# Optimization experiments

Hardware: AMD Instinct MI355X
Metric: run time of the kernel (lower is better)

## Reference

```python
import jax, jax.numpy as jnp
import numpy as np

D_MODEL = 1024
NUM_HEADS = 16
D_K = D_MODEL // NUM_HEADS
B, S = 2, 2048


def setup_inputs() -> dict:
    key = jax.random.key(0)
    ks = jax.random.split(key, 12)
    s = 1.0 / np.sqrt(D_MODEL)
    return {
        "query": jax.random.normal(ks[0], (B, S, D_MODEL), jnp.float32),
        "key": jax.random.normal(ks[1], (B, S, D_MODEL), jnp.float32),
        "value": jax.random.normal(ks[2], (B, S, D_MODEL), jnp.float32),
        "mask": jnp.ones((B, S), jnp.int32),
        "Wq": jax.random.uniform(ks[3], (D_MODEL, D_MODEL), jnp.float32, -s, s),
        "bq": jax.random.uniform(ks[4], (D_MODEL,), jnp.float32, -s, s),
        "Wk": jax.random.uniform(ks[5], (D_MODEL, D_MODEL), jnp.float32, -s, s),
        "bk": jax.random.uniform(ks[6], (D_MODEL,), jnp.float32, -s, s),
        "Wv": jax.random.uniform(ks[7], (D_MODEL, D_MODEL), jnp.float32, -s, s),
        "bv": jax.random.uniform(ks[8], (D_MODEL,), jnp.float32, -s, s),
        "Wo": jax.random.uniform(ks[9], (D_MODEL, D_MODEL), jnp.float32, -s, s),
        "bo": jax.random.uniform(ks[10], (D_MODEL,), jnp.float32, -s, s),
    }


def reference(query, key, value, mask, Wq, bq, Wk, bk, Wv, bv, Wo, bo):
    b, s, _ = query.shape
    scale = jnp.sqrt(jnp.asarray(D_K, jnp.float32)).astype(query.dtype)
    # QKV projections: x @ W.T + b (torch nn.Linear convention)
    Q = (query @ Wq.T + bq).reshape(b, s, NUM_HEADS, D_K).transpose(0, 2, 1, 3)
    K = (key @ Wk.T + bk).reshape(b, -1, NUM_HEADS, D_K).transpose(0, 2, 1, 3)
    V = (value @ Wv.T + bv).reshape(b, -1, NUM_HEADS, D_K).transpose(0, 2, 1, 3)
    # scores in fp32, then cast back to input dtype (matches source)
    scores = jnp.einsum('bhqd,bhkd->bhqk', Q.astype(jnp.float32), K.astype(jnp.float32)) / scale
    scores = scores.astype(Q.dtype)
    # 2D mask [B,S] -> [B,1,1,S], broadcast over heads/queries
    fill = jnp.finfo(scores.dtype).min
    scores = jnp.where(mask[:, None, None, :] == 0, fill, scores)
    attn = jax.nn.softmax(scores, axis=-1)  # dropout p=0 -> identity
    context = jnp.einsum('bhqk,bhkd->bhqd', attn, V)
    context = context.transpose(0, 2, 1, 3).reshape(b, s, D_MODEL)
    return context @ Wo.T + bo
```

## Files before the change

kernel.cpp:

```cpp
#include <hip/hip_runtime.h>


typedef __bf16 bf16_8 __attribute__((ext_vector_type(8)));
typedef float  f32x4  __attribute__((ext_vector_type(4)));
typedef float  f32x16 __attribute__((ext_vector_type(16)));
typedef unsigned int u32x4 __attribute__((ext_vector_type(4)));

#define MFMA16(a, b, c) __builtin_amdgcn_mfma_f32_16x16x32_bf16((a), (b), (c), 0, 0, 0)
#define MFMA32(a, b, c) __builtin_amdgcn_mfma_f32_32x32x16_bf16((a), (b), (c), 0, 0, 0)

__device__ __forceinline__ void async_ld16(const void* g, void* l) {
  __builtin_amdgcn_global_load_lds(
      (__attribute__((address_space(1))) void*)g,
      (__attribute__((address_space(3))) void*)l, 16, 0, 0);
}

__device__ __forceinline__ void gemm_core_128(
    const __bf16* __restrict__ A, const __bf16* __restrict__ BT, int K,
    int tm, int tn, __bf16* At, __bf16* Bt, f32x4 acc[4][4]) {
  const int tid  = threadIdx.x;
  const int lane = tid & 63;
  const int w    = tid >> 6;
  const int quad = lane >> 4;
  const int c16  = lane & 15;
  const int wm = w >> 1, wn = w & 1;

  const int ch0  = w * 2;
  const int row0 = ch0 * 16 + (lane >> 2);
  const int col0 = (lane & 3) * 8;
  const __bf16* Ag = A  + (size_t)(tm + row0) * K + col0;
  const __bf16* Bg = BT + (size_t)(tn + row0) * K + col0;
  __bf16* Al = At + ch0 * 512;
  __bf16* Bl = Bt + ch0 * 512;
  const size_t rowK16 = (size_t)16 * K;

  for (int kt = 0; kt < K; kt += 32) {
    async_ld16(Ag + kt,          Al);
    async_ld16(Ag + rowK16 + kt, Al + 512);
    async_ld16(Bg + kt,          Bl);
    async_ld16(Bg + rowK16 + kt, Bl + 512);
    __syncthreads();

    bf16_8 af[4], bfr[4];
#pragma unroll
    for (int mi = 0; mi < 4; ++mi)
      af[mi] = *(const bf16_8*)(At + (wm * 64 + mi * 16 + c16) * 32 + quad * 8);
#pragma unroll
    for (int ni = 0; ni < 4; ++ni)
      bfr[ni] = *(const bf16_8*)(Bt + (wn * 64 + ni * 16 + c16) * 32 + quad * 8);
#pragma unroll
    for (int mi = 0; mi < 4; ++mi)
#pragma unroll
      for (int ni = 0; ni < 4; ++ni)
        acc[mi][ni] = MFMA16(af[mi], bfr[ni], acc[mi][ni]);
    __syncthreads();
  }
}

__global__ __launch_bounds__(256)
void qkv_fused(const __bf16* __restrict__ xq, const __bf16* __restrict__ xk,
               const __bf16* __restrict__ xv,
               const __bf16* __restrict__ wq, const __bf16* __restrict__ wk,
               const __bf16* __restrict__ wv,
               const float* __restrict__ bq, const float* __restrict__ bk,
               const float* __restrict__ bv,
               __bf16* __restrict__ Qo, __bf16* __restrict__ Ko,
               __bf16* __restrict__ Vo) {
  __shared__ __bf16 At[128 * 32];
  __shared__ __bf16 Bt[128 * 32];
  const int z  = blockIdx.z;
  const int bx = blockIdx.x;
  const __bf16 *A, *BT;
  const float* bias;
  int tm, tn;
  if (z == 2) {
    A = wv; BT = xv; bias = bv;
    tm = (bx >> 5) * 128; tn = (bx & 31) * 128;
  } else if (z == 1) {
    A = xk; BT = wk; bias = bk;
    tm = (bx >> 3) * 128; tn = (bx & 7) * 128;
  } else {
    A = xq; BT = wq; bias = bq;
    tm = (bx >> 3) * 128; tn = (bx & 7) * 128;
  }

  f32x4 acc[4][4];
  const f32x4 zero4 = {0.f, 0.f, 0.f, 0.f};
#pragma unroll
  for (int i = 0; i < 4; ++i)
#pragma unroll
    for (int j = 0; j < 4; ++j) acc[i][j] = zero4;

  gemm_core_128(A, BT, 1024, tm, tn, At, Bt, acc);

  const int lane = threadIdx.x & 63;
  const int w    = threadIdx.x >> 6;
  const int quad = lane >> 4, c16 = lane & 15;
  const int wm = w >> 1, wn = w & 1;

  if (z == 2) {
#pragma unroll
    for (int mi = 0; mi < 4; ++mi) {
#pragma unroll
      for (int ni = 0; ni < 4; ++ni) {
        const int n  = tn + wn * 64 + ni * 16 + c16;
        const int bb = n >> 11, s = n & 2047;
#pragma unroll
        for (int r = 0; r < 4; ++r) {
          const int m  = tm + wm * 64 + mi * 16 + quad * 4 + r;
          const int hh = m >> 6, d = m & 63;
          Vo[(((size_t)(bb * 16 + hh) * 64 + d) << 11) + s] =
              (__bf16)(acc[mi][ni][r] + bias[m]);
        }
      }
    }
  } else {
    __bf16* Out = (z == 1) ? Ko : Qo;
    const float scale = (z == 0) ? 0.125f : 1.0f;
#pragma unroll
    for (int mi = 0; mi < 4; ++mi) {
#pragma unroll
      for (int ni = 0; ni < 4; ++ni) {
        const int n  = tn + wn * 64 + ni * 16 + c16;
        const int hh = n >> 6, d = n & 63;
        const float bn = bias[n];
#pragma unroll
        for (int r = 0; r < 4; ++r) {
          const int m  = tm + wm * 64 + mi * 16 + quad * 4 + r;
          const int bb = m >> 11, s = m & 2047;
          Out[(((size_t)(bb * 16 + hh) * 2048 + s) << 6) + d] =
              (__bf16)((acc[mi][ni][r] + bn) * scale);
        }
      }
    }
  }
}

__global__ __launch_bounds__(256)
void out_proj(const __bf16* __restrict__ ctx, const __bf16* __restrict__ wo,
              const float* __restrict__ bo, float* __restrict__ out) {
  __shared__ __bf16 At[64 * 32];
  __shared__ __bf16 Bt[128 * 32];
  const int bx = blockIdx.x;
  const int tm = (bx >> 3) * 64, tn = (bx & 7) * 128;

  const int tid  = threadIdx.x;
  const int lane = tid & 63, w = tid >> 6;
  const int quad = lane >> 4, c16 = lane & 15;
  const int wm = w >> 1, wn = w & 1;

  const int row0 = lane >> 2, col0 = (lane & 3) * 8;
  const __bf16* Ag = ctx + (size_t)(tm + w * 16 + row0) * 1024 + col0;
  const __bf16* Bg = wo  + (size_t)(tn + w * 32 + row0) * 1024 + col0;
  __bf16* Al = At + w * 512;
  __bf16* Bl = Bt + w * 1024;

  f32x4 acc[2][4];
  const f32x4 zero4 = {0.f, 0.f, 0.f, 0.f};
#pragma unroll
  for (int i = 0; i < 2; ++i)
#pragma unroll
    for (int j = 0; j < 4; ++j) acc[i][j] = zero4;

  for (int kt = 0; kt < 1024; kt += 32) {
    async_ld16(Ag + kt, Al);
    async_ld16(Bg + kt, Bl);
    async_ld16(Bg + 16 * 1024 + kt, Bl + 512);
    __syncthreads();

    bf16_8 af[2], bfr[4];
#pragma unroll
    for (int mi = 0; mi < 2; ++mi)
      af[mi] = *(const bf16_8*)(At + (wm * 32 + mi * 16 + c16) * 32 + quad * 8);
#pragma unroll
    for (int ni = 0; ni < 4; ++ni)
      bfr[ni] = *(const bf16_8*)(Bt + (wn * 64 + ni * 16 + c16) * 32 + quad * 8);
#pragma unroll
    for (int mi = 0; mi < 2; ++mi)
#pragma unroll
      for (int ni = 0; ni < 4; ++ni)
        acc[mi][ni] = MFMA16(af[mi], bfr[ni], acc[mi][ni]);
    __syncthreads();
  }

#pragma unroll
  for (int mi = 0; mi < 2; ++mi) {
#pragma unroll
    for (int ni = 0; ni < 4; ++ni) {
      const int n = tn + wn * 64 + ni * 16 + c16;
      const float bn = bo[n];
#pragma unroll
      for (int r = 0; r < 4; ++r) {
        const int m = tm + wm * 32 + mi * 16 + quad * 4 + r;
        out[(size_t)m * 1024 + n] = acc[mi][ni][r] + bn;
      }
    }
  }
}

__global__ __launch_bounds__(512, 4)
void flash_attn(const __bf16* __restrict__ Qg, const __bf16* __restrict__ Kg,
                const __bf16* __restrict__ VTg, const int* __restrict__ maskg,
                __bf16* __restrict__ ctx) {
  __shared__ __align__(16) __bf16 Kl[2][64 * 72];
  __shared__ __align__(16) __bf16 Vl[2][64 * 72];
  __shared__ __align__(16) float  maskadd[2][64];
  __shared__ __align__(16) float  Om[4][32][64];
  __shared__ float Lm[4][32];

  const int t    = threadIdx.x;
  const int lane = t & 63;
  const int w    = t >> 6;
  const int g    = w & 3;
  const int hh   = w >> 2;
  const int n32  = lane & 31;
  const int h    = lane >> 5;

  const int linear = blockIdx.x + (blockIdx.y << 4) + (blockIdx.z << 8);
  const int sw     = (linear & 7) * 64 + (linear >> 3);
  const int qt     = sw & 15;
  const int head   = (sw >> 4) & 15;
  const int b      = sw >> 8;

  const size_t bh = (size_t)(b * 16 + head);
  const int qbase = qt * 128 + g * 32;

  bf16_8 bq[4];
  {
    const __bf16* qptr = Qg + (bh * 2048 + qbase + n32) * 64 + h * 8;
#pragma unroll
    for (int s = 0; s < 4; ++s) bq[s] = *(const bf16_8*)(qptr + s * 16);
  }

  const f32x16 z16 = {0.f,0.f,0.f,0.f,0.f,0.f,0.f,0.f,
                      0.f,0.f,0.f,0.f,0.f,0.f,0.f,0.f};
  f32x16 o0 = z16, o1 = z16;
  float lsum = 0.f;

  const int tl   = t & 255;
  const int srow = tl >> 2, scc = (tl & 3) * 16;
  const __bf16* Kgp = Kg  + (bh * 2048 + hh * 1024) * 64;
  const __bf16* Vgp = VTg + bh * 64 * 2048 + hh * 1024;
  const int*    mgp = maskg + b * 2048 + hh * 1024;
  const float LOG2E = 1.44269504088896f;

  for (int kt = 0; kt < 1024; kt += 64) {
    {
      const size_t kb = (size_t)(kt + srow) * 64 + scc;
      *(bf16_8*)&Kl[hh][srow * 72 + scc]     = *(const bf16_8*)&Kgp[kb];
      *(bf16_8*)&Kl[hh][srow * 72 + scc + 8] = *(const bf16_8*)&Kgp[kb + 8];
      const size_t vbi = (size_t)srow * 2048 + kt + scc;
      *(bf16_8*)&Vl[hh][srow * 72 + scc]     = *(const bf16_8*)&Vgp[vbi];
      *(bf16_8*)&Vl[hh][srow * 72 + scc + 8] = *(const bf16_8*)&Vgp[vbi + 8];
      if (tl < 64) maskadd[hh][tl] = mgp[kt + tl] ? -17.3123404907f : -1e30f;
    }
    __syncthreads();

#pragma unroll
    for (int kt2 = 0; kt2 < 2; ++kt2) {
      f32x16 p = z16;
#pragma unroll
      for (int s = 0; s < 4; ++s) {
        const bf16_8 ka =
            *(const bf16_8*)&Kl[hh][(kt2 * 32 + n32) * 72 + s * 16 + h * 8];
        p = MFMA32(ka, bq[s], p);
      }
      unsigned c[8];
#pragma unroll
      for (int i = 0; i < 8; ++i) {
        const int r0 = 2 * i, r1 = 2 * i + 1;
        const float ma0 =
            maskadd[hh][kt2 * 32 + (r0 & 3) + 8 * (r0 >> 2) + 4 * h];
        const float ma1 =
            maskadd[hh][kt2 * 32 + (r1 & 3) + 8 * (r1 >> 2) + 4 * h];
        const float e0 = __builtin_amdgcn_exp2f(fmaf(p[r0], LOG2E, ma0));
        const float e1 = __builtin_amdgcn_exp2f(fmaf(p[r1], LOG2E, ma1));
        lsum += e0 + e1;
        union { __bf16 hx[2]; unsigned u; } uu;
        uu.hx[0] = (__bf16)e0;
        uu.hx[1] = (__bf16)e1;
        c[i] = uu.u;
      }
      asm volatile("v_permlane32_swap_b32 %0, %1" : "+v"(c[0]), "+v"(c[2]));
      asm volatile("v_permlane32_swap_b32 %0, %1" : "+v"(c[1]), "+v"(c[3]));
      asm volatile("v_permlane32_swap_b32 %0, %1" : "+v"(c[4]), "+v"(c[6]));
      asm volatile("v_permlane32_swap_b32 %0, %1" : "+v"(c[5]), "+v"(c[7]));
#pragma unroll
      for (int sub = 0; sub < 2; ++sub) {
        const u32x4 av = {c[4 * sub + 0], c[4 * sub + 1],
                          c[4 * sub + 2], c[4 * sub + 3]};
        const bf16_8 aP = __builtin_bit_cast(bf16_8, av);
        const int s = kt2 * 2 + sub;
        const bf16_8 vb0 =
            *(const bf16_8*)&Vl[hh][n32 * 72 + s * 16 + h * 8];
        const bf16_8 vb1 =
            *(const bf16_8*)&Vl[hh][(32 + n32) * 72 + s * 16 + h * 8];
        o0 = MFMA32(aP, vb0, o0);
        o1 = MFMA32(aP, vb1, o1);
      }
    }
    __syncthreads();
  }

  lsum += __shfl_xor(lsum, 32);

  if (hh) {
#pragma unroll
    for (int r = 0; r < 16; ++r) {
      const int qrow = (r & 3) + 8 * (r >> 2) + 4 * h;
      Om[g][qrow][n32]      = o0[r];
      Om[g][qrow][32 + n32] = o1[r];
    }
    if (h == 0) Lm[g][n32] = lsum;
  }
  __syncthreads();
  if (!hh) {
    const float linv = 1.0f / (lsum + Lm[g][n32]);
#pragma unroll
    for (int r = 0; r < 16; ++r) {
      const int qrow = (r & 3) + 8 * (r >> 2) + 4 * h;
      const float li = __shfl(linv, qrow);
      __bf16* cp = ctx + ((size_t)b * 2048 + qbase + qrow) * 1024 + head * 64;
      cp[n32]      = (__bf16)((o0[r] + Om[g][qrow][n32]) * li);
      cp[32 + n32] = (__bf16)((o1[r] + Om[g][qrow][32 + n32]) * li);
    }
  }
}

__global__ __launch_bounds__(256)
void cvt_all(const float* __restrict__ q, const float* __restrict__ k,
             const float* __restrict__ v, const float* __restrict__ Wq,
             const float* __restrict__ Wk, const float* __restrict__ Wv,
             const float* __restrict__ Wo,
             __bf16* __restrict__ xq, __bf16* __restrict__ xk,
             __bf16* __restrict__ xv, __bf16* __restrict__ wqb,
             __bf16* __restrict__ wkb, __bf16* __restrict__ wvb,
             __bf16* __restrict__ wob) {
  const int y = blockIdx.y;
  const float* s;
  __bf16* d;
  int n8;
  switch (y) {
    case 0: s = q;  d = xq;  n8 = 524288; break;
    case 1: s = k;  d = xk;  n8 = 524288; break;
    case 2: s = v;  d = xv;  n8 = 524288; break;
    case 3: s = Wq; d = wqb; n8 = 131072; break;
    case 4: s = Wk; d = wkb; n8 = 131072; break;
    case 5: s = Wv; d = wvb; n8 = 131072; break;
    default: s = Wo; d = wob; n8 = 131072; break;
  }
  const int i = blockIdx.x * blockDim.x + threadIdx.x;
  if (i < n8) {
    const float4* sp = (const float4*)s;
    const float4 v0 = sp[i * 2], v1 = sp[i * 2 + 1];
    bf16_8 o;
    o[0] = (__bf16)v0.x; o[1] = (__bf16)v0.y;
    o[2] = (__bf16)v0.z; o[3] = (__bf16)v0.w;
    o[4] = (__bf16)v1.x; o[5] = (__bf16)v1.y;
    o[6] = (__bf16)v1.z; o[7] = (__bf16)v1.w;
    *(bf16_8*)(d + (size_t)i * 8) = o;
  }
}

extern "C" void kernel_launch(void* const* d_in, const int* in_sizes, int n_in,
                              void* d_out, int out_size, void* d_ws, size_t ws_size,
                              hipStream_t stream) {
  (void)in_sizes; (void)n_in; (void)out_size; (void)ws_size;
  const float* q    = (const float*)d_in[0];
  const float* k    = (const float*)d_in[1];
  const float* v    = (const float*)d_in[2];
  const int*   mask = (const int*)d_in[3];
  const float* Wq = (const float*)d_in[4];
  const float* bq = (const float*)d_in[5];
  const float* Wk = (const float*)d_in[6];
  const float* bk = (const float*)d_in[7];
  const float* Wv = (const float*)d_in[8];
  const float* bv = (const float*)d_in[9];
  const float* Wo = (const float*)d_in[10];
  const float* bo = (const float*)d_in[11];

  char* ws = (char*)d_ws;
  const size_t MB = 1ull << 20;
  __bf16* xq  = (__bf16*)(ws + 0 * MB);
  __bf16* xk  = (__bf16*)(ws + 8 * MB);
  __bf16* xv  = (__bf16*)(ws + 16 * MB);
  __bf16* wqb = (__bf16*)(ws + 24 * MB);
  __bf16* wkb = (__bf16*)(ws + 26 * MB);
  __bf16* wvb = (__bf16*)(ws + 28 * MB);
  __bf16* wob = (__bf16*)(ws + 30 * MB);
  __bf16* Qb  = (__bf16*)(ws + 32 * MB);
  __bf16* Kb  = (__bf16*)(ws + 40 * MB);
  __bf16* VTb = (__bf16*)(ws + 48 * MB);
  __bf16* ctx = (__bf16*)(ws + 56 * MB);

  cvt_all<<<dim3(2048, 7), 256, 0, stream>>>(q, k, v, Wq, Wk, Wv, Wo,
                                             xq, xk, xv, wqb, wkb, wvb, wob);

  qkv_fused<<<dim3(256, 1, 3), 256, 0, stream>>>(xq, xk, xv, wqb, wkb, wvb,
                                                 bq, bk, bv, Qb, Kb, VTb);

  flash_attn<<<dim3(16, 16, 2), 512, 0, stream>>>(Qb, Kb, VTb, mask, ctx);

  out_proj<<<dim3(512), 256, 0, stream>>>(ctx, wob, bo, (float*)d_out);
}
```

Before: 221.4 us.

## Double-buffer flash attention K/V tiles with register prefetch and one barrier

```diff
diff --git a/kernel.cpp b/kernel.cpp
--- a/kernel.cpp
+++ b/kernel.cpp
@@ -202,11 +202,7 @@
 void flash_attn(const __bf16* __restrict__ Qg, const __bf16* __restrict__ Kg,
                 const __bf16* __restrict__ VTg, const int* __restrict__ maskg,
                 __bf16* __restrict__ ctx) {
-  __shared__ __align__(16) __bf16 Kl[2][64 * 72];
-  __shared__ __align__(16) __bf16 Vl[2][64 * 72];
-  __shared__ __align__(16) float  maskadd[2][64];
-  __shared__ __align__(16) float  Om[4][32][64];
-  __shared__ float Lm[4][32];
+  __shared__ __align__(16) char smem_[76288];
 
   const int t    = threadIdx.x;
   const int lane = t & 63;
@@ -244,37 +240,69 @@
   const int*    mgp = maskg + b * 2048 + hh * 1024;
   const float LOG2E = 1.44269504088896f;
 
-  for (int kt = 0; kt < 1024; kt += 64) {
+  __bf16* const Kb0 = (__bf16*)smem_;
+  __bf16* const Vb0 = (__bf16*)(smem_ + 36864);
+  float*  const Mb0 = (float*)(smem_ + 73728);
+
+  bf16_8 rk0, rk1, rv0, rv1;
+  int rmv;
+
+#define FA_ISSUE(KT) do {                                         \
+    const size_t kb_ = (size_t)((KT) + srow) * 64 + scc;          \
+    rk0 = *(const bf16_8*)&Kgp[kb_];                              \
+    rk1 = *(const bf16_8*)&Kgp[kb_ + 8];                          \
+    const size_t vb_ = (size_t)srow * 2048 + (KT) + scc;          \
+    rv0 = *(const bf16_8*)&Vgp[vb_];                              \
+    rv1 = *(const bf16_8*)&Vgp[vb_ + 8];                          \
+    if (tl < 64) rmv = mgp[(KT) + tl];                            \
+  } while (0)
+
+  FA_ISSUE(0);
+
+  for (int it = 0; it < 16; ++it) {
+    const int cur = it & 1;
+    __bf16* const Klc = Kb0 + (cur * 2 + hh) * 4608;
+    __bf16* const Vlc = Vb0 + (cur * 2 + hh) * 4608;
+    float*  const Mlc = Mb0 + (cur * 2 + hh) * 64;
+
     {
-      const size_t kb = (size_t)(kt + srow) * 64 + scc;
-      *(bf16_8*)&Kl[hh][srow * 72 + scc]     = *(const bf16_8*)&Kgp[kb];
-      *(bf16_8*)&Kl[hh][srow * 72 + scc + 8] = *(const bf16_8*)&Kgp[kb + 8];
-      const size_t vbi = (size_t)srow * 2048 + kt + scc;
-      *(bf16_8*)&Vl[hh][srow * 72 + scc]     = *(const bf16_8*)&Vgp[vbi];
-      *(bf16_8*)&Vl[hh][srow * 72 + scc + 8] = *(const bf16_8*)&Vgp[vbi + 8];
-      if (tl < 64) maskadd[hh][tl] = mgp[kt + tl] ? -17.3123404907f : -1e30f;
-    }
+      __bf16* kw = Klc + srow * 72 + scc;
+      *(bf16_8*)kw       = rk0;
+      *(bf16_8*)(kw + 8) = rk1;
+      __bf16* vw = Vlc + srow * 72 + scc;
+      *(bf16_8*)vw       = rv0;
+      *(bf16_8*)(vw + 8) = rv1;
+      if (tl < 64) Mlc[tl] = rmv ? -17.3123404907f : -1e30f;
+    }
+    if (it + 1 < 16) FA_ISSUE((it + 1) * 64);
+
     __syncthreads();
 
 #pragma unroll
     for (int kt2 = 0; kt2 < 2; ++kt2) {
+      f32x4 ma4[4];
+#pragma unroll
+      for (int j = 0; j < 4; ++j)
+        ma4[j] = *(const f32x4*)&Mlc[kt2 * 32 + 8 * j + 4 * h];
+
       f32x16 p = z16;
+      __builtin_amdgcn_s_setprio(1);
 #pragma unroll
       for (int s = 0; s < 4; ++s) {
         const bf16_8 ka =
-            *(const bf16_8*)&Kl[hh][(kt2 * 32 + n32) * 72 + s * 16 + h * 8];
+            *(const bf16_8*)&Klc[(kt2 * 32 + n32) * 72 + s * 16 + h * 8];
         p = MFMA32(ka, bq[s], p);
       }
+      __builtin_amdgcn_s_setprio(0);
+
       unsigned c[8];
 #pragma unroll
       for (int i = 0; i < 8; ++i) {
         const int r0 = 2 * i, r1 = 2 * i + 1;
-        const float ma0 =
-            maskadd[hh][kt2 * 32 + (r0 & 3) + 8 * (r0 >> 2) + 4 * h];
-        const float ma1 =
-            maskadd[hh][kt2 * 32 + (r1 & 3) + 8 * (r1 >> 2) + 4 * h];
-        const float e0 = __builtin_amdgcn_exp2f(fmaf(p[r0], LOG2E, ma0));
-        const float e1 = __builtin_amdgcn_exp2f(fmaf(p[r1], LOG2E, ma1));
+        const float e0 =
+            __builtin_amdgcn_exp2f(fmaf(p[r0], LOG2E, ma4[r0 >> 2][r0 & 3]));
+        const float e1 =
+            __builtin_amdgcn_exp2f(fmaf(p[r1], LOG2E, ma4[r1 >> 2][r1 & 3]));
         lsum += e0 + e1;
         union { __bf16 hx[2]; unsigned u; } uu;
         uu.hx[0] = (__bf16)e0;
@@ -285,6 +313,7 @@
       asm volatile("v_permlane32_swap_b32 %0, %1" : "+v"(c[1]), "+v"(c[3]));
       asm volatile("v_permlane32_swap_b32 %0, %1" : "+v"(c[4]), "+v"(c[6]));
       asm volatile("v_permlane32_swap_b32 %0, %1" : "+v"(c[5]), "+v"(c[7]));
+
 #pragma unroll
       for (int sub = 0; sub < 2; ++sub) {
         const u32x4 av = {c[4 * sub + 0], c[4 * sub + 1],
@@ -292,17 +321,24 @@
         const bf16_8 aP = __builtin_bit_cast(bf16_8, av);
         const int s = kt2 * 2 + sub;
         const bf16_8 vb0 =
-            *(const bf16_8*)&Vl[hh][n32 * 72 + s * 16 + h * 8];
+            *(const bf16_8*)&Vlc[n32 * 72 + s * 16 + h * 8];
         const bf16_8 vb1 =
-            *(const bf16_8*)&Vl[hh][(32 + n32) * 72 + s * 16 + h * 8];
+            *(const bf16_8*)&Vlc[(32 + n32) * 72 + s * 16 + h * 8];
+        __builtin_amdgcn_s_setprio(1);
         o0 = MFMA32(aP, vb0, o0);
         o1 = MFMA32(aP, vb1, o1);
-      }
-    }
-    __syncthreads();
-  }
+        __builtin_amdgcn_s_setprio(0);
+      }
+    }
+  }
+#undef FA_ISSUE
 
   lsum += __shfl_xor(lsum, 32);
+
+  __syncthreads();
+
+  float (*Om)[32][64] = (float(*)[32][64])smem_;
+  float (*Lm)[32]     = (float(*)[32])(smem_ + 75776);
 
   if (hh) {
 #pragma unroll
```

Measured after the change: 221.0 us. No clear change (-0.2%).

## Drop LDS staging in flash attention, load K/V directly, fold scale into Q

Applied to the files above, without the earlier changes.

```diff
diff --git a/kernel.cpp b/kernel.cpp
--- a/kernel.cpp
+++ b/kernel.cpp
@@ -116,7 +116,7 @@
     }
   } else {
     __bf16* Out = (z == 1) ? Ko : Qo;
-    const float scale = (z == 0) ? 0.125f : 1.0f;
+    const float scale = (z == 0) ? 0.1803368801f : 1.0f;
 #pragma unroll
     for (int mi = 0; mi < 4; ++mi) {
 #pragma unroll
@@ -198,32 +198,29 @@
   }
 }
 
-__global__ __launch_bounds__(512, 4)
+__global__ __launch_bounds__(256, 4)
 void flash_attn(const __bf16* __restrict__ Qg, const __bf16* __restrict__ Kg,
-                const __bf16* __restrict__ VTg, const int* __restrict__ maskg,
+                const __bf16* __restrict__ VTg, const float* __restrict__ maskf,
                 __bf16* __restrict__ ctx) {
-  __shared__ __align__(16) __bf16 Kl[2][64 * 72];
-  __shared__ __align__(16) __bf16 Vl[2][64 * 72];
-  __shared__ __align__(16) float  maskadd[2][64];
-  __shared__ __align__(16) float  Om[4][32][64];
-  __shared__ float Lm[4][32];
+  __shared__ __align__(16) float Om[2][32][64];
+  __shared__ float Lm[2][32];
 
   const int t    = threadIdx.x;
   const int lane = t & 63;
   const int w    = t >> 6;
-  const int g    = w & 3;
-  const int hh   = w >> 2;
+  const int g    = w & 1;
+  const int hh   = w >> 1;
   const int n32  = lane & 31;
   const int h    = lane >> 5;
 
-  const int linear = blockIdx.x + (blockIdx.y << 4) + (blockIdx.z << 8);
-  const int sw     = (linear & 7) * 64 + (linear >> 3);
-  const int qt     = sw & 15;
-  const int head   = (sw >> 4) & 15;
-  const int b      = sw >> 8;
+  const int linear = blockIdx.x + (blockIdx.y << 5) + (blockIdx.z << 9);
+  const int sw     = (linear & 7) * 128 + (linear >> 3);
+  const int qt     = sw & 31;
+  const int head   = (sw >> 5) & 15;
+  const int b      = sw >> 9;
 
   const size_t bh = (size_t)(b * 16 + head);
-  const int qbase = qt * 128 + g * 32;
+  const int qbase = qt * 64 + g * 32;
 
   bf16_8 bq[4];
   {
@@ -237,69 +234,59 @@
   f32x16 o0 = z16, o1 = z16;
   float lsum = 0.f;
 
-  const int tl   = t & 255;
-  const int srow = tl >> 2, scc = (tl & 3) * 16;
-  const __bf16* Kgp = Kg  + (bh * 2048 + hh * 1024) * 64;
-  const __bf16* Vgp = VTg + bh * 64 * 2048 + hh * 1024;
-  const int*    mgp = maskg + b * 2048 + hh * 1024;
-  const float LOG2E = 1.44269504088896f;
-
-  for (int kt = 0; kt < 1024; kt += 64) {
-    {
-      const size_t kb = (size_t)(kt + srow) * 64 + scc;
-      *(bf16_8*)&Kl[hh][srow * 72 + scc]     = *(const bf16_8*)&Kgp[kb];
-      *(bf16_8*)&Kl[hh][srow * 72 + scc + 8] = *(const bf16_8*)&Kgp[kb + 8];
-      const size_t vbi = (size_t)srow * 2048 + kt + scc;
-      *(bf16_8*)&Vl[hh][srow * 72 + scc]     = *(const bf16_8*)&Vgp[vbi];
-      *(bf16_8*)&Vl[hh][srow * 72 + scc + 8] = *(const bf16_8*)&Vgp[vbi + 8];
-      if (tl < 64) maskadd[hh][tl] = mgp[kt + tl] ? -17.3123404907f : -1e30f;
-    }
-    __syncthreads();
-
-#pragma unroll
-    for (int kt2 = 0; kt2 < 2; ++kt2) {
-      f32x16 p = z16;
-#pragma unroll
-      for (int s = 0; s < 4; ++s) {
-        const bf16_8 ka =
-            *(const bf16_8*)&Kl[hh][(kt2 * 32 + n32) * 72 + s * 16 + h * 8];
-        p = MFMA32(ka, bq[s], p);
-      }
-      unsigned c[8];
-#pragma unroll
-      for (int i = 0; i < 8; ++i) {
-        const int r0 = 2 * i, r1 = 2 * i + 1;
-        const float ma0 =
-            maskadd[hh][kt2 * 32 + (r0 & 3) + 8 * (r0 >> 2) + 4 * h];
-        const float ma1 =
-            maskadd[hh][kt2 * 32 + (r1 & 3) + 8 * (r1 >> 2) + 4 * h];
-        const float e0 = __builtin_amdgcn_exp2f(fmaf(p[r0], LOG2E, ma0));
-        const float e1 = __builtin_amdgcn_exp2f(fmaf(p[r1], LOG2E, ma1));
-        lsum += e0 + e1;
-        union { __bf16 hx[2]; unsigned u; } uu;
-        uu.hx[0] = (__bf16)e0;
-        uu.hx[1] = (__bf16)e1;
-        c[i] = uu.u;
-      }
-      asm volatile("v_permlane32_swap_b32 %0, %1" : "+v"(c[0]), "+v"(c[2]));
-      asm volatile("v_permlane32_swap_b32 %0, %1" : "+v"(c[1]), "+v"(c[3]));
-      asm volatile("v_permlane32_swap_b32 %0, %1" : "+v"(c[4]), "+v"(c[6]));
-      asm volatile("v_permlane32_swap_b32 %0, %1" : "+v"(c[5]), "+v"(c[7]));
-#pragma unroll
-      for (int sub = 0; sub < 2; ++sub) {
-        const u32x4 av = {c[4 * sub + 0], c[4 * sub + 1],
-                          c[4 * sub + 2], c[4 * sub + 3]};
-        const bf16_8 aP = __builtin_bit_cast(bf16_8, av);
-        const int s = kt2 * 2 + sub;
-        const bf16_8 vb0 =
-            *(const bf16_8*)&Vl[hh][n32 * 72 + s * 16 + h * 8];
-        const bf16_8 vb1 =
-            *(const bf16_8*)&Vl[hh][(32 + n32) * 72 + s * 16 + h * 8];
-        o0 = MFMA32(aP, vb0, o0);
-        o1 = MFMA32(aP, vb1, o1);
-      }
-    }
-    __syncthreads();
+  const __bf16* kS  = Kg  + (bh * 2048 + hh * 1024 + n32) * 64 + h * 8;
+  const __bf16* vS0 = VTg + (bh * 64 + n32) * 2048 + hh * 1024 + h * 8;
+  const __bf16* vS1 = vS0 + 32 * 2048;
+  const float*  mS  = maskf + b * 2048 + hh * 1024 + 4 * h;
+
+#pragma unroll 2
+  for (int it = 0; it < 32; ++it) {
+    f32x16 p;
+#pragma unroll
+    for (int j = 0; j < 4; ++j) {
+      const f32x4 m4 = *(const f32x4*)(mS + 8 * j);
+      p[4 * j + 0] = m4[0];
+      p[4 * j + 1] = m4[1];
+      p[4 * j + 2] = m4[2];
+      p[4 * j + 3] = m4[3];
+    }
+#pragma unroll
+    for (int s = 0; s < 4; ++s) {
+      const bf16_8 ka = *(const bf16_8*)(kS + s * 16);
+      p = MFMA32(ka, bq[s], p);
+    }
+
+    unsigned c[8];
+#pragma unroll
+    for (int i = 0; i < 8; ++i) {
+      const float e0 = __builtin_amdgcn_exp2f(p[2 * i]);
+      const float e1 = __builtin_amdgcn_exp2f(p[2 * i + 1]);
+      lsum += e0 + e1;
+      union { __bf16 hx[2]; unsigned u; } uu;
+      uu.hx[0] = (__bf16)e0;
+      uu.hx[1] = (__bf16)e1;
+      c[i] = uu.u;
+    }
+    asm volatile("v_permlane32_swap_b32 %0, %1" : "+v"(c[0]), "+v"(c[2]));
+    asm volatile("v_permlane32_swap_b32 %0, %1" : "+v"(c[1]), "+v"(c[3]));
+    asm volatile("v_permlane32_swap_b32 %0, %1" : "+v"(c[4]), "+v"(c[6]));
+    asm volatile("v_permlane32_swap_b32 %0, %1" : "+v"(c[5]), "+v"(c[7]));
+
+#pragma unroll
+    for (int sub = 0; sub < 2; ++sub) {
+      const u32x4 av = {c[4 * sub + 0], c[4 * sub + 1],
+                        c[4 * sub + 2], c[4 * sub + 3]};
+      const bf16_8 aP = __builtin_bit_cast(bf16_8, av);
+      const bf16_8 vb0 = *(const bf16_8*)(vS0 + sub * 16);
+      const bf16_8 vb1 = *(const bf16_8*)(vS1 + sub * 16);
+      o0 = MFMA32(aP, vb0, o0);
+      o1 = MFMA32(aP, vb1, o1);
+    }
+
+    kS  += 32 * 64;
+    vS0 += 32;
+    vS1 += 32;
+    mS  += 32;
   }
 
   lsum += __shfl_xor(lsum, 32);
@@ -331,12 +318,17 @@
 void cvt_all(const float* __restrict__ q, const float* __restrict__ k,
              const float* __restrict__ v, const float* __restrict__ Wq,
              const float* __restrict__ Wk, const float* __restrict__ Wv,
-             const float* __restrict__ Wo,
+             const float* __restrict__ Wo, const int* __restrict__ mask,
              __bf16* __restrict__ xq, __bf16* __restrict__ xk,
              __bf16* __restrict__ xv, __bf16* __restrict__ wqb,
              __bf16* __restrict__ wkb, __bf16* __restrict__ wvb,
-             __bf16* __restrict__ wob) {
+             __bf16* __restrict__ wob, float* __restrict__ maskf) {
   const int y = blockIdx.y;
+  const int i = blockIdx.x * blockDim.x + threadIdx.x;
+  if (y == 7) {
+    if (i < 4096) maskf[i] = mask[i] ? -17.3123404907f : -1e30f;
+    return;
+  }
   const float* s;
   __bf16* d;
   int n8;
@@ -349,7 +341,6 @@
     case 5: s = Wv; d = wvb; n8 = 131072; break;
     default: s = Wo; d = wob; n8 = 131072; break;
   }
-  const int i = blockIdx.x * blockDim.x + threadIdx.x;
   if (i < n8) {
     const float4* sp = (const float4*)s;
     const float4 v0 = sp[i * 2], v1 = sp[i * 2 + 1];
@@ -392,14 +383,16 @@
   __bf16* Kb  = (__bf16*)(ws + 40 * MB);
   __bf16* VTb = (__bf16*)(ws + 48 * MB);
   __bf16* ctx = (__bf16*)(ws + 56 * MB);
-
-  cvt_all<<<dim3(2048, 7), 256, 0, stream>>>(q, k, v, Wq, Wk, Wv, Wo,
-                                             xq, xk, xv, wqb, wkb, wvb, wob);
+  float*  maskf = (float*)(ws + 70 * MB);
+
+  cvt_all<<<dim3(2048, 8), 256, 0, stream>>>(q, k, v, Wq, Wk, Wv, Wo, mask,
+                                             xq, xk, xv, wqb, wkb, wvb, wob,
+                                             maskf);
 
   qkv_fused<<<dim3(256, 1, 3), 256, 0, stream>>>(xq, xk, xv, wqb, wkb, wvb,
                                                  bq, bk, bv, Qb, Kb, VTb);
 
-  flash_attn<<<dim3(16, 16, 2), 512, 0, stream>>>(Qb, Kb, VTb, mask, ctx);
+  flash_attn<<<dim3(32, 16, 2), 256, 0, stream>>>(Qb, Kb, VTb, maskf, ctx);
 
   out_proj<<<dim3(512), 256, 0, stream>>>(ctx, wob, bo, (float*)d_out);
 }
```

New measurement: 306.5 us. +38.4%, slower.

## Fold log2e into Q scale, seed MFMA accumulator with mask, enlarge K/V tile

Applied to the files above, without the earlier changes.

```diff
diff --git a/kernel.cpp b/kernel.cpp
--- a/kernel.cpp
+++ b/kernel.cpp
@@ -116,7 +116,7 @@
     }
   } else {
     __bf16* Out = (z == 1) ? Ko : Qo;
-    const float scale = (z == 0) ? 0.125f : 1.0f;
+    const float scale = (z == 0) ? 0.1803368801f : 1.0f;
 #pragma unroll
     for (int mi = 0; mi < 4; ++mi) {
 #pragma unroll
@@ -202,11 +202,7 @@
 void flash_attn(const __bf16* __restrict__ Qg, const __bf16* __restrict__ Kg,
                 const __bf16* __restrict__ VTg, const int* __restrict__ maskg,
                 __bf16* __restrict__ ctx) {
-  __shared__ __align__(16) __bf16 Kl[2][64 * 72];
-  __shared__ __align__(16) __bf16 Vl[2][64 * 72];
-  __shared__ __align__(16) float  maskadd[2][64];
-  __shared__ __align__(16) float  Om[4][32][64];
-  __shared__ float Lm[4][32];
+  __shared__ __align__(16) char smem_[73216];
 
   const int t    = threadIdx.x;
   const int lane = t & 63;
@@ -237,44 +233,54 @@
   f32x16 o0 = z16, o1 = z16;
   float lsum = 0.f;
 
+  __bf16* const Kl = (__bf16*)smem_           + hh * (128 * 72);
+  __bf16* const Vl = (__bf16*)(smem_ + 36864) + hh * (64 * 136);
+  float*  const Ml = (float*)(smem_ + 71680)  + hh * 128;
+
   const int tl   = t & 255;
   const int srow = tl >> 2, scc = (tl & 3) * 16;
   const __bf16* Kgp = Kg  + (bh * 2048 + hh * 1024) * 64;
   const __bf16* Vgp = VTg + bh * 64 * 2048 + hh * 1024;
   const int*    mgp = maskg + b * 2048 + hh * 1024;
-  const float LOG2E = 1.44269504088896f;
-
-  for (int kt = 0; kt < 1024; kt += 64) {
-    {
-      const size_t kb = (size_t)(kt + srow) * 64 + scc;
-      *(bf16_8*)&Kl[hh][srow * 72 + scc]     = *(const bf16_8*)&Kgp[kb];
-      *(bf16_8*)&Kl[hh][srow * 72 + scc + 8] = *(const bf16_8*)&Kgp[kb + 8];
-      const size_t vbi = (size_t)srow * 2048 + kt + scc;
-      *(bf16_8*)&Vl[hh][srow * 72 + scc]     = *(const bf16_8*)&Vgp[vbi];
-      *(bf16_8*)&Vl[hh][srow * 72 + scc + 8] = *(const bf16_8*)&Vgp[vbi + 8];
-      if (tl < 64) maskadd[hh][tl] = mgp[kt + tl] ? -17.3123404907f : -1e30f;
-    }
-    __syncthreads();
-
-#pragma unroll
-    for (int kt2 = 0; kt2 < 2; ++kt2) {
-      f32x16 p = z16;
+
+  for (int ktb = 0; ktb < 1024; ktb += 128) {
+#pragma unroll
+    for (int r2 = 0; r2 < 2; ++r2) {
+      const size_t kb = (size_t)(ktb + r2 * 64 + srow) * 64 + scc;
+      __bf16* kw = Kl + (r2 * 64 + srow) * 72 + scc;
+      *(bf16_8*)kw       = *(const bf16_8*)&Kgp[kb];
+      *(bf16_8*)(kw + 8) = *(const bf16_8*)&Kgp[kb + 8];
+      const size_t vb = (size_t)srow * 2048 + ktb + r2 * 64 + scc;
+      __bf16* vw = Vl + srow * 136 + r2 * 64 + scc;
+      *(bf16_8*)vw       = *(const bf16_8*)&Vgp[vb];
+      *(bf16_8*)(vw + 8) = *(const bf16_8*)&Vgp[vb + 8];
+    }
+    if (tl < 128) Ml[tl] = mgp[ktb + tl] ? -17.3123404907f : -1e30f;
+    __syncthreads();
+
+#pragma unroll
+    for (int kt2 = 0; kt2 < 4; ++kt2) {
+      f32x16 p;
+#pragma unroll
+      for (int j = 0; j < 4; ++j) {
+        const f32x4 m4 = *(const f32x4*)&Ml[kt2 * 32 + 8 * j + 4 * h];
+        p[4 * j + 0] = m4[0];
+        p[4 * j + 1] = m4[1];
+        p[4 * j + 2] = m4[2];
+        p[4 * j + 3] = m4[3];
+      }
 #pragma unroll
       for (int s = 0; s < 4; ++s) {
         const bf16_8 ka =
-            *(const bf16_8*)&Kl[hh][(kt2 * 32 + n32) * 72 + s * 16 + h * 8];
+            *(const bf16_8*)&Kl[(kt2 * 32 + n32) * 72 + s * 16 + h * 8];
         p = MFMA32(ka, bq[s], p);
       }
+
       unsigned c[8];
 #pragma unroll
       for (int i = 0; i < 8; ++i) {
-        const int r0 = 2 * i, r1 = 2 * i + 1;
-        const float ma0 =
-            maskadd[hh][kt2 * 32 + (r0 & 3) + 8 * (r0 >> 2) + 4 * h];
-        const float ma1 =
-            maskadd[hh][kt2 * 32 + (r1 & 3) + 8 * (r1 >> 2) + 4 * h];
-        const float e0 = __builtin_amdgcn_exp2f(fmaf(p[r0], LOG2E, ma0));
-        const float e1 = __builtin_amdgcn_exp2f(fmaf(p[r1], LOG2E, ma1));
+        const float e0 = __builtin_amdgcn_exp2f(p[2 * i]);
+        const float e1 = __builtin_amdgcn_exp2f(p[2 * i + 1]);
         lsum += e0 + e1;
         union { __bf16 hx[2]; unsigned u; } uu;
         uu.hx[0] = (__bf16)e0;
@@ -285,6 +291,7 @@
       asm volatile("v_permlane32_swap_b32 %0, %1" : "+v"(c[1]), "+v"(c[3]));
       asm volatile("v_permlane32_swap_b32 %0, %1" : "+v"(c[4]), "+v"(c[6]));
       asm volatile("v_permlane32_swap_b32 %0, %1" : "+v"(c[5]), "+v"(c[7]));
+
 #pragma unroll
       for (int sub = 0; sub < 2; ++sub) {
         const u32x4 av = {c[4 * sub + 0], c[4 * sub + 1],
@@ -292,9 +299,9 @@
         const bf16_8 aP = __builtin_bit_cast(bf16_8, av);
         const int s = kt2 * 2 + sub;
         const bf16_8 vb0 =
-            *(const bf16_8*)&Vl[hh][n32 * 72 + s * 16 + h * 8];
+            *(const bf16_8*)&Vl[n32 * 136 + s * 16 + h * 8];
         const bf16_8 vb1 =
-            *(const bf16_8*)&Vl[hh][(32 + n32) * 72 + s * 16 + h * 8];
+            *(const bf16_8*)&Vl[(32 + n32) * 136 + s * 16 + h * 8];
         o0 = MFMA32(aP, vb0, o0);
         o1 = MFMA32(aP, vb1, o1);
       }
@@ -303,6 +310,9 @@
   }
 
   lsum += __shfl_xor(lsum, 32);
+
+  float (*Om)[32][64] = (float(*)[32][64])smem_;
+  float (*Lm)[32]     = (float(*)[32])(smem_ + 72704);
 
   if (hh) {
 #pragma unroll
```

Result: no change. 220.9 us (-0.3%).
